# Kernel optimization log

Measured on AMD Instinct MI355X. Metric: run time of the kernel, lower is better.

Reference implementation:

```python
import jax, jax.numpy as jnp
import numpy as np

NUM_HEADS = 16  # init_kwargs num_heads


def setup_inputs() -> dict:
    key = jax.random.key(0)
    ks = jax.random.split(key, 3)
    B, S, D = 4, 2048, 1024
    scale = 1.0 / np.sqrt(D)
    return {
        "x": jax.random.normal(ks[0], (B, S, D), dtype=jnp.float32),
        "in_proj_w": jax.random.normal(ks[1], (3 * D, D), dtype=jnp.float32) * scale,
        "in_proj_b": jnp.zeros((3 * D,), dtype=jnp.float32),
        "out_w": jax.random.normal(ks[2], (D, D), dtype=jnp.float32) * scale,
        "out_b": jnp.zeros((D,), dtype=jnp.float32),
        "gamma": jnp.ones((D,), dtype=jnp.float32),
        "beta": jnp.zeros((D,), dtype=jnp.float32),
    }


def reference(x, in_proj_w, in_proj_b, out_w, out_b, gamma, beta):
    B, S, D = x.shape
    H = NUM_HEADS
    hd = D // H
    # packed qkv projection (torch Linear convention: y = x @ W.T + b)
    qkv = x @ in_proj_w.T + in_proj_b            # [B,S,3D]
    q, k, v = jnp.split(qkv, 3, axis=-1)
    q = q.reshape(B, S, H, hd).transpose(0, 2, 1, 3)  # [B,H,S,hd]
    k = k.reshape(B, S, H, hd).transpose(0, 2, 1, 3)
    v = v.reshape(B, S, H, hd).transpose(0, 2, 1, 3)

    scores = jnp.einsum("bhqd,bhkd->bhqk", q, k) / jnp.sqrt(jnp.asarray(hd, x.dtype))
    # additive causal mask: -inf above the diagonal
    causal = jnp.tril(jnp.ones((S, S), dtype=bool))
    scores = jnp.where(causal, scores, jnp.asarray(-jnp.inf, scores.dtype))
    attn = jax.nn.softmax(scores, axis=-1)       # [B,H,S,S]

    ctx = jnp.einsum("bhqk,bhkd->bhqd", attn, v)  # [B,H,S,hd]
    ctx = ctx.transpose(0, 2, 1, 3).reshape(B, S, D)
    attn_out = ctx @ out_w.T + out_b

    y = x + attn_out
    mu = jnp.mean(y, axis=-1, keepdims=True)
    var = jnp.mean(jnp.square(y - mu), axis=-1, keepdims=True)
    y = (y - mu) * jax.lax.rsqrt(var + 1e-5) * gamma + beta
    return y
```

## Files before the change

### kernel.cpp

```cpp
#include <hip/hip_runtime.h>
#include <stdint.h>

typedef unsigned short u16;
typedef __bf16 bf16x8 __attribute__((ext_vector_type(8)));
typedef float  f32x4  __attribute__((ext_vector_type(4)));
typedef int    i32x4  __attribute__((ext_vector_type(4)));

__device__ __forceinline__ u16 f2bf(float f){
  union{float f; uint32_t u;} v; v.f = f;
  uint32_t r = v.u + 0x7FFFu + ((v.u >> 16) & 1u);
  return (u16)(r >> 16);
}

#define GLDS16(gp, lp) __builtin_amdgcn_global_load_lds( \
    (const __attribute__((address_space(1))) void*)(gp),  \
    (__attribute__((address_space(3))) void*)(lp), 16, 0, 0)

__global__ __launch_bounds__(256) void cvt_kernel(const float* __restrict__ in,
                                                  u16* __restrict__ out, int n4) {
  int stride = gridDim.x * blockDim.x;
  for (int i = blockIdx.x * blockDim.x + threadIdx.x; i < n4; i += stride) {
    float4 v = ((const float4*)in)[i];
    u16 o0 = f2bf(v.x), o1 = f2bf(v.y), o2 = f2bf(v.z), o3 = f2bf(v.w);
    u16* p = out + (size_t)i * 4;
    uint32_t lo = (uint32_t)o0 | ((uint32_t)o1 << 16);
    uint32_t hi = (uint32_t)o2 | ((uint32_t)o3 << 16);
    ((uint2*)p)[0] = make_uint2(lo, hi);
  }
}

template <int MODE>
__global__ __launch_bounds__(256) void gemm_bt(
    const u16* __restrict__ A, const u16* __restrict__ B,
    const float* __restrict__ bias,
    u16* __restrict__ Cbf, float* __restrict__ Cf, const float* __restrict__ resid,
    int M, int N, int K) {
  __shared__ u16 Alds[128 * 32];
  __shared__ u16 Blds[128 * 32];
  const int t = threadIdx.x;
  const int w = t >> 6, l = t & 63;
  const int wr = w >> 1, wc = w & 1;
  const int g = l >> 4, r16 = l & 15;
  const int brow = blockIdx.y * 128, bcol = blockIdx.x * 128;

  f32x4 acc[4][4];
#pragma unroll
  for (int mi = 0; mi < 4; mi++)
#pragma unroll
    for (int nj = 0; nj < 4; nj++) acc[mi][nj] = (f32x4){0.f, 0.f, 0.f, 0.f};

  const int c0 = 2 * w, c1 = 2 * w + 1;
  const int srow0 = c0 * 16 + (l >> 2);
  const int srow1 = c1 * 16 + (l >> 2);
  const int scol = (l & 3) * 8;

  for (int kt = 0; kt < K; kt += 32) {
    __syncthreads();
    GLDS16(A + (size_t)(brow + srow0) * K + kt + scol, (char*)Alds + c0 * 1024);
    GLDS16(A + (size_t)(brow + srow1) * K + kt + scol, (char*)Alds + c1 * 1024);
    GLDS16(B + (size_t)(bcol + srow0) * K + kt + scol, (char*)Blds + c0 * 1024);
    GLDS16(B + (size_t)(bcol + srow1) * K + kt + scol, (char*)Blds + c1 * 1024);
    __syncthreads();

    bf16x8 af[4], bfr[4];
#pragma unroll
    for (int mi = 0; mi < 4; mi++)
      af[mi] = *(const bf16x8*)&Alds[(wr * 64 + mi * 16 + r16) * 32 + g * 8];
#pragma unroll
    for (int nj = 0; nj < 4; nj++)
      bfr[nj] = *(const bf16x8*)&Blds[(wc * 64 + nj * 16 + r16) * 32 + g * 8];
#pragma unroll
    for (int mi = 0; mi < 4; mi++)
#pragma unroll
      for (int nj = 0; nj < 4; nj++)
        acc[mi][nj] = __builtin_amdgcn_mfma_f32_16x16x32_bf16(af[mi], bfr[nj], acc[mi][nj], 0, 0, 0);
  }

#pragma unroll
  for (int mi = 0; mi < 4; mi++) {
#pragma unroll
    for (int nj = 0; nj < 4; nj++) {
      int col = bcol + wc * 64 + nj * 16 + r16;
      float bv = bias[col];
#pragma unroll
      for (int rr = 0; rr < 4; rr++) {
        int row = brow + wr * 64 + mi * 16 + g * 4 + rr;
        float v = acc[mi][nj][rr] + bv;
        if (MODE == 0) {
          Cbf[(size_t)row * N + col] = f2bf(v);
        } else {
          v += resid[(size_t)row * N + col];
          Cf[(size_t)row * N + col] = v;
        }
      }
    }
  }
}

__global__ __launch_bounds__(256) void vtrans_kernel(const u16* __restrict__ qkv,
                                                     u16* __restrict__ vtg) {
  const int S = 2048, HD3 = 3072;
  __shared__ u16 Vs[64 * 64];
  const int st = blockIdx.x, h = blockIdx.y, b = blockIdx.z;
  const int t = threadIdx.x;
  const int s0 = st * 64;
#pragma unroll
  for (int i = 0; i < 2; i++) {
    int n = t + i * 256;
    int row = n >> 3, c = n & 7;
    const u16* src = qkv + ((size_t)(b * S) + s0 + row) * HD3 + 2048 + h * 64 + c * 8;
    i32x4 v = *(const i32x4*)src;
    *(i32x4*)&Vs[row * 64 + ((c ^ (row & 7)) << 3)] = v;
  }
  __syncthreads();
  const int d = t >> 2;
  const int dc = d >> 3, dl = d & 7;
#pragma unroll
  for (int i = 0; i < 2; i++) {
    int kc = (t & 3) + i * 4;
    u16 tmp[8];
#pragma unroll
    for (int j = 0; j < 8; j++) {
      int k = kc * 8 + j;
      tmp[j] = Vs[k * 64 + ((dc ^ (k & 7)) << 3) + dl];
    }
    *(i32x4*)(vtg + ((size_t)(b * 16 + h) * 64 + d) * S + s0 + kc * 8) = *(i32x4*)tmp;
  }
}

__global__ __launch_bounds__(256) void attn_kernel(const u16* __restrict__ qkv,
                                                   const u16* __restrict__ vtg,
                                                   u16* __restrict__ ctxb) {
  const int S = 2048, HD3 = 3072;
  __shared__ u16 Kl[2][64 * 64];
  __shared__ u16 Vl[2][64 * 64];
  __shared__ u16 Pb[4][16 * 64];

  const int qi = 15 - (int)blockIdx.y;
  const int h = blockIdx.x & 15, b = blockIdx.x >> 4;
  const int t = threadIdx.x, w = t >> 6, l = t & 63;
  const int g = l >> 4, r16 = l & 15;
  const int q0 = qi * 128;
  const int nt = 2 * qi + 2;
  const size_t bS = (size_t)b * S;
  const size_t vbase = ((size_t)(b * 16 + h)) * 64 * S;

  const int q0w = q0 + w * 32;
  bf16x8 qf[2][2];
#pragma unroll
  for (int hh = 0; hh < 2; hh++) {
    const u16* qp = qkv + (bS + q0w + hh * 16 + r16) * HD3 + h * 64 + g * 8;
    qf[hh][0] = *(const bf16x8*)qp;
    qf[hh][1] = *(const bf16x8*)(qp + 32);
  }

  f32x4 ctx[2][4];
#pragma unroll
  for (int hh = 0; hh < 2; hh++)
#pragma unroll
    for (int f = 0; f < 4; f++) ctx[hh][f] = (f32x4){0.f, 0.f, 0.f, 0.f};
  float mrun[2] = {-1e30f, -1e30f};
  float lrun[2] = {0.f, 0.f};

#define STAGE(kt_, bi_)                                                        \
  do {                                                                         \
    const int k0s = (kt_) * 64;                                                \
    _Pragma("unroll")                                                          \
    for (int c = 0; c < 2; c++) {                                              \
      int n = c * 256 + t;                                                     \
      int row = n >> 3, sl = n & 7;                                            \
      int col = ((sl ^ (row & 7)) << 3);                                       \
      GLDS16(qkv + (bS + k0s + row) * HD3 + 1024 + h * 64 + col,               \
             (char*)&Kl[bi_][0] + c * 4096 + w * 1024);                        \
      GLDS16(vtg + vbase + (size_t)row * S + k0s + col,                        \
             (char*)&Vl[bi_][0] + c * 4096 + w * 1024);                        \
    }                                                                          \
  } while (0)

  STAGE(0, 0);
  int cur = 0;
  for (int kt = 0; kt < nt; kt++) {
    const int k0 = kt * 64;
    asm volatile("s_waitcnt vmcnt(0)" ::: "memory");
    __syncthreads();
    if (kt + 1 < nt) STAGE(kt + 1, cur ^ 1);

    bf16x8 kf[4][2];
#pragma unroll
    for (int f = 0; f < 4; f++) {
      int row = f * 16 + r16;
#pragma unroll
      for (int c = 0; c < 2; c++)
        kf[f][c] = *(const bf16x8*)&Kl[cur][row * 64 + (((c * 4 + g) ^ (row & 7)) << 3)];
    }

#pragma unroll
    for (int hh = 0; hh < 2; hh++) {
      const int qmin = q0w + hh * 16;
      if (k0 >= qmin + 16) continue;

      f32x4 sf[4];
#pragma unroll
      for (int f = 0; f < 4; f++) {
        f32x4 s = (f32x4){0.f, 0.f, 0.f, 0.f};
        s = __builtin_amdgcn_mfma_f32_16x16x32_bf16(kf[f][0], qf[hh][0], s, 0, 0, 0);
        s = __builtin_amdgcn_mfma_f32_16x16x32_bf16(kf[f][1], qf[hh][1], s, 0, 0, 0);
        sf[f] = s * 0.125f;
      }
      const int qg = qmin + r16;
      if (k0 + 64 > qmin) {
#pragma unroll
        for (int f = 0; f < 4; f++)
#pragma unroll
          for (int rr = 0; rr < 4; rr++)
            if (k0 + f * 16 + g * 4 + rr > qg) sf[f][rr] = -1e30f;
      }

      float tm = sf[0][0];
#pragma unroll
      for (int f = 0; f < 4; f++)
#pragma unroll
        for (int rr = 0; rr < 4; rr++) tm = fmaxf(tm, sf[f][rr]);
      tm = fmaxf(tm, __shfl_xor(tm, 16, 64));
      tm = fmaxf(tm, __shfl_xor(tm, 32, 64));

      float mold = mrun[hh];
      float mnew = fmaxf(mold, tm);
      mrun[hh] = mnew;

      float p[4][4];
      float ps = 0.f;
#pragma unroll
      for (int f = 0; f < 4; f++)
#pragma unroll
        for (int rr = 0; rr < 4; rr++) {
          p[f][rr] = __expf(sf[f][rr] - mnew);
          ps += p[f][rr];
        }
      ps += __shfl_xor(ps, 16, 64);
      ps += __shfl_xor(ps, 32, 64);
      float sc = __expf(mold - mnew);
      lrun[hh] = lrun[hh] * sc + ps;

#pragma unroll
      for (int f = 0; f < 4; f++)
#pragma unroll
        for (int rr2 = 0; rr2 < 4; rr2 += 2) {
          union { __bf16 b; u16 u; } a0, a1;
          a0.b = (__bf16)p[f][rr2];
          a1.b = (__bf16)p[f][rr2 + 1];
          uint32_t pk = (uint32_t)a0.u | ((uint32_t)a1.u << 16);
          int kidx = f * 16 + g * 4 + rr2;
          int ch = kidx >> 3;
          *(uint32_t*)((char*)&Pb[w][0] + r16 * 128 + ((ch ^ (r16 & 7)) << 4) +
                       ((kidx & 7) << 1)) = pk;
        }

#pragma unroll
      for (int rr = 0; rr < 4; rr++) {
        float scq = __shfl(sc, g * 4 + rr, 64);
#pragma unroll
        for (int f = 0; f < 4; f++) ctx[hh][f][rr] *= scq;
      }

      bf16x8 pf[2];
#pragma unroll
      for (int kh = 0; kh < 2; kh++)
        pf[kh] = *(const bf16x8*)((char*)&Pb[w][0] + r16 * 128 +
                                  (((kh * 4 + g) ^ (r16 & 7)) << 4));
#pragma unroll
      for (int f = 0; f < 4; f++) {
        int row = f * 16 + r16;
#pragma unroll
        for (int kh = 0; kh < 2; kh++) {
          bf16x8 vf = *(const bf16x8*)&Vl[cur][row * 64 + (((kh * 4 + g) ^ (row & 7)) << 3)];
          ctx[hh][f] = __builtin_amdgcn_mfma_f32_16x16x32_bf16(pf[kh], vf, ctx[hh][f], 0, 0, 0);
        }
      }
    }
    cur ^= 1;
  }

#pragma unroll
  for (int hh = 0; hh < 2; hh++) {
    float linv = 1.f / lrun[hh];
#pragma unroll
    for (int rr = 0; rr < 4; rr++) {
      float li = __shfl(linv, g * 4 + rr, 64);
      int qg = q0w + hh * 16 + g * 4 + rr;
#pragma unroll
      for (int f = 0; f < 4; f++) {
        union { __bf16 b; u16 u; } o;
        o.b = (__bf16)(ctx[hh][f][rr] * li);
        ctxb[(bS + qg) * 1024 + h * 64 + f * 16 + r16] = o.u;
      }
    }
  }
#undef STAGE
}

__global__ __launch_bounds__(256) void ln_kernel(float* __restrict__ y,
                                                 const float* __restrict__ gamma,
                                                 const float* __restrict__ beta) {
  __shared__ float sh[4];
  const int row = blockIdx.x, t = threadIdx.x;
  const int w = t >> 6, l = t & 63;
  float4 v = ((const float4*)(y + (size_t)row * 1024))[t];
  float s = v.x + v.y + v.z + v.w;
#pragma unroll
  for (int m = 32; m; m >>= 1) s += __shfl_xor(s, m, 64);
  if (l == 0) sh[w] = s;
  __syncthreads();
  float mu = (sh[0] + sh[1] + sh[2] + sh[3]) * (1.0f / 1024.0f);
  float dx = v.x - mu, dy = v.y - mu, dz = v.z - mu, dw = v.w - mu;
  float ss = dx * dx + dy * dy + dz * dz + dw * dw;
#pragma unroll
  for (int m = 32; m; m >>= 1) ss += __shfl_xor(ss, m, 64);
  __syncthreads();
  if (l == 0) sh[w] = ss;
  __syncthreads();
  float var = (sh[0] + sh[1] + sh[2] + sh[3]) * (1.0f / 1024.0f);
  float rs = rsqrtf(var + 1e-5f);
  float4 gm = ((const float4*)gamma)[t];
  float4 bt = ((const float4*)beta)[t];
  float4 o;
  o.x = dx * rs * gm.x + bt.x;
  o.y = dy * rs * gm.y + bt.y;
  o.z = dz * rs * gm.z + bt.z;
  o.w = dw * rs * gm.w + bt.w;
  ((float4*)(y + (size_t)row * 1024))[t] = o;
}

extern "C" void kernel_launch(void* const* d_in, const int* in_sizes, int n_in,
                              void* d_out, int out_size, void* d_ws, size_t ws_size,
                              hipStream_t stream) {
  (void)in_sizes; (void)n_in; (void)out_size; (void)ws_size;
  const float* x     = (const float*)d_in[0];
  const float* w1    = (const float*)d_in[1];
  const float* b1    = (const float*)d_in[2];
  const float* w2    = (const float*)d_in[3];
  const float* b2    = (const float*)d_in[4];
  const float* gamma = (const float*)d_in[5];
  const float* beta  = (const float*)d_in[6];
  float* out = (float*)d_out;

  const int M = 8192, D = 1024, N1 = 3072;

  char* ws = (char*)d_ws;
  u16* x_bf   = (u16*)(ws);
  u16* w1_bf  = (u16*)(ws + 16777216);
  u16* w2_bf  = (u16*)(ws + 23068672);
  u16* qkv_bf = (u16*)(ws + 25165824);
  u16* ctx_bf = (u16*)(ws + 75497472);
  u16* vtg    = (u16*)(ws);

  cvt_kernel<<<2048, 256, 0, stream>>>(x, x_bf, M * D / 4);
  cvt_kernel<<<1024, 256, 0, stream>>>(w1, w1_bf, N1 * D / 4);
  cvt_kernel<<<512, 256, 0, stream>>>(w2, w2_bf, D * D / 4);

  gemm_bt<0><<<dim3(N1 / 128, M / 128), 256, 0, stream>>>(
      x_bf, w1_bf, b1, qkv_bf, nullptr, nullptr, M, N1, D);

  vtrans_kernel<<<dim3(32, 16, 4), 256, 0, stream>>>(qkv_bf, vtg);

  attn_kernel<<<dim3(64, 16), 256, 0, stream>>>(qkv_bf, vtg, ctx_bf);

  gemm_bt<1><<<dim3(D / 128, M / 128), 256, 0, stream>>>(
      ctx_bf, w2_bf, b2, nullptr, out, x, M, D, D);

  ln_kernel<<<M, 256, 0, stream>>>(out, gamma, beta);
}
```

Measured before the change: 321.7 us.

## Pair causal query tiles per block, fold scale into Q, skip rescale, swizzle GEMM tiles

The attention grid is halved, and each block now processes two query tiles (pair and 15-pair) so causal work is balanced across blocks. The softmax scale and log2e are folded into Q once, so the loop can use exp2f. Rescaling of the accumulator is skipped when the running max grows by less than 8 (FA4-style lazy rescale). LDS offsets are precomputed, and the GEMM block index is XCD-swizzled for better L2 locality. Together these cut tail imbalance and per-tile ALU work, at the cost of extra bf16 rounding of Q and possible loss of fp32 headroom in the lazy-rescale path.

```diff
diff --git a/kernel.cpp b/kernel.cpp
--- a/kernel.cpp
+++ b/kernel.cpp
@@ -41,7 +41,13 @@
   const int w = t >> 6, l = t & 63;
   const int wr = w >> 1, wc = w & 1;
   const int g = l >> 4, r16 = l & 15;
-  const int brow = blockIdx.y * 128, bcol = blockIdx.x * 128;
+
+  const int gx = gridDim.x;
+  const int nwg = gx * gridDim.y;
+  const int wg = blockIdx.y * gx + blockIdx.x;
+  const int cpx = nwg >> 3;
+  const int swz = (wg & 7) * cpx + (wg >> 3);
+  const int brow = (swz / gx) * 128, bcol = (swz % gx) * 128;
 
   f32x4 acc[4][4];
 #pragma unroll
@@ -136,163 +142,190 @@
   __shared__ u16 Vl[2][64 * 64];
   __shared__ u16 Pb[4][16 * 64];
 
-  const int qi = 15 - (int)blockIdx.y;
   const int h = blockIdx.x & 15, b = blockIdx.x >> 4;
+  const int pair = blockIdx.y;
   const int t = threadIdx.x, w = t >> 6, l = t & 63;
   const int g = l >> 4, r16 = l & 15;
-  const int q0 = qi * 128;
-  const int nt = 2 * qi + 2;
   const size_t bS = (size_t)b * S;
   const size_t vbase = ((size_t)(b * 16 + h)) * 64 * S;
 
-  const int q0w = q0 + w * 32;
-  bf16x8 qf[2][2];
-#pragma unroll
-  for (int hh = 0; hh < 2; hh++) {
-    const u16* qp = qkv + (bS + q0w + hh * 16 + r16) * HD3 + h * 64 + g * 8;
-    qf[hh][0] = *(const bf16x8*)qp;
-    qf[hh][1] = *(const bf16x8*)(qp + 32);
-  }
-
-  f32x4 ctx[2][4];
-#pragma unroll
-  for (int hh = 0; hh < 2; hh++)
-#pragma unroll
-    for (int f = 0; f < 4; f++) ctx[hh][f] = (f32x4){0.f, 0.f, 0.f, 0.f};
-  float mrun[2] = {-1e30f, -1e30f};
-  float lrun[2] = {0.f, 0.f};
-
-#define STAGE(kt_, bi_)                                                        \
-  do {                                                                         \
-    const int k0s = (kt_) * 64;                                                \
-    _Pragma("unroll")                                                          \
-    for (int c = 0; c < 2; c++) {                                              \
-      int n = c * 256 + t;                                                     \
-      int row = n >> 3, sl = n & 7;                                            \
-      int col = ((sl ^ (row & 7)) << 3);                                       \
-      GLDS16(qkv + (bS + k0s + row) * HD3 + 1024 + h * 64 + col,               \
-             (char*)&Kl[bi_][0] + c * 4096 + w * 1024);                        \
-      GLDS16(vtg + vbase + (size_t)row * S + k0s + col,                        \
-             (char*)&Vl[bi_][0] + c * 4096 + w * 1024);                        \
-    }                                                                          \
+  const int srow = t >> 3, ssl = t & 7;
+  const int scol = ((ssl ^ (srow & 7)) << 3);
+  const int sdst = w * 1024;
+
+  int kfo[4][2], pwo[4][2], pro[2];
+#pragma unroll
+  for (int f = 0; f < 4; f++) {
+    int row = f * 16 + r16;
+#pragma unroll
+    for (int c = 0; c < 2; c++)
+      kfo[f][c] = (row * 64 + (((c * 4 + g) ^ (row & 7)) << 3)) * 2;
+#pragma unroll
+    for (int q2 = 0; q2 < 2; q2++) {
+      int kidx = f * 16 + g * 4 + q2 * 2;
+      pwo[f][q2] = r16 * 128 + (((kidx >> 3) ^ (r16 & 7)) << 4) + ((kidx & 7) << 1);
+    }
+  }
+#pragma unroll
+  for (int kh = 0; kh < 2; kh++)
+    pro[kh] = r16 * 128 + (((kh * 4 + g) ^ (r16 & 7)) << 4);
+
+  const float QSC = 0.125f * 1.44269504f;
+
+#define STAGE(bi_)                                                            \
+  do {                                                                        \
+    GLDS16(kp, (char*)Kl + (bi_)*8192 + sdst);                                \
+    GLDS16(kp + 32 * HD3, (char*)Kl + (bi_)*8192 + 4096 + sdst);              \
+    GLDS16(vp, (char*)Vl + (bi_)*8192 + sdst);                                \
+    GLDS16(vp + 32 * S, (char*)Vl + (bi_)*8192 + 4096 + sdst);                \
+    kp += 64 * HD3; vp += 64;                                                 \
   } while (0)
 
-  STAGE(0, 0);
-  int cur = 0;
-  for (int kt = 0; kt < nt; kt++) {
-    const int k0 = kt * 64;
-    asm volatile("s_waitcnt vmcnt(0)" ::: "memory");
+  for (int seg = 0; seg < 2; seg++) {
+    const int qi = seg ? (15 - pair) : pair;
+    const int q0w = qi * 128 + w * 32;
+    const int nt = 2 * qi + 2;
+
+    bf16x8 qf[2][2];
+#pragma unroll
+    for (int hh = 0; hh < 2; hh++) {
+      const u16* qp = qkv + (bS + q0w + hh * 16 + r16) * HD3 + h * 64 + g * 8;
+      bf16x8 a = *(const bf16x8*)qp;
+      bf16x8 c = *(const bf16x8*)(qp + 32);
+#pragma unroll
+      for (int j = 0; j < 8; j++) {
+        a[j] = (__bf16)((float)a[j] * QSC);
+        c[j] = (__bf16)((float)c[j] * QSC);
+      }
+      qf[hh][0] = a; qf[hh][1] = c;
+    }
+
+    f32x4 ctx[2][4];
+#pragma unroll
+    for (int hh = 0; hh < 2; hh++)
+#pragma unroll
+      for (int f = 0; f < 4; f++) ctx[hh][f] = (f32x4){0.f, 0.f, 0.f, 0.f};
+    float mrun[2] = {-1e30f, -1e30f};
+    float lrun[2] = {0.f, 0.f};
+
+    const u16* kp = qkv + (bS + srow) * HD3 + 1024 + h * 64 + scol;
+    const u16* vp = vtg + vbase + (size_t)srow * S + scol;
+
     __syncthreads();
-    if (kt + 1 < nt) STAGE(kt + 1, cur ^ 1);
-
-    bf16x8 kf[4][2];
-#pragma unroll
-    for (int f = 0; f < 4; f++) {
-      int row = f * 16 + r16;
-#pragma unroll
-      for (int c = 0; c < 2; c++)
-        kf[f][c] = *(const bf16x8*)&Kl[cur][row * 64 + (((c * 4 + g) ^ (row & 7)) << 3)];
+    STAGE(0);
+    int cur = 0;
+    for (int kt = 0; kt < nt; kt++) {
+      const int k0 = kt * 64;
+      asm volatile("s_waitcnt vmcnt(0)" ::: "memory");
+      __syncthreads();
+      if (kt + 1 < nt) STAGE(cur ^ 1);
+
+      const char* KB = (const char*)Kl + cur * 8192;
+      const char* VB = (const char*)Vl + cur * 8192;
+      bf16x8 kf[4][2];
+#pragma unroll
+      for (int f = 0; f < 4; f++)
+#pragma unroll
+        for (int c = 0; c < 2; c++) kf[f][c] = *(const bf16x8*)(KB + kfo[f][c]);
+
+#pragma unroll
+      for (int hh = 0; hh < 2; hh++) {
+        const int qmin = q0w + hh * 16;
+        if (k0 >= qmin + 16) continue;
+
+        f32x4 sf[4];
+#pragma unroll
+        for (int f = 0; f < 4; f++) {
+          f32x4 s = (f32x4){0.f, 0.f, 0.f, 0.f};
+          s = __builtin_amdgcn_mfma_f32_16x16x32_bf16(kf[f][0], qf[hh][0], s, 0, 0, 0);
+          s = __builtin_amdgcn_mfma_f32_16x16x32_bf16(kf[f][1], qf[hh][1], s, 0, 0, 0);
+          sf[f] = s;
+        }
+        const int qg = qmin + r16;
+        if (k0 + 64 > qmin) {
+#pragma unroll
+          for (int f = 0; f < 4; f++)
+#pragma unroll
+            for (int rr = 0; rr < 4; rr++)
+              if (k0 + f * 16 + g * 4 + rr > qg) sf[f][rr] = -1e30f;
+        }
+
+        float tm = sf[0][0];
+#pragma unroll
+        for (int f = 0; f < 4; f++)
+#pragma unroll
+          for (int rr = 0; rr < 4; rr++) tm = fmaxf(tm, sf[f][rr]);
+        tm = fmaxf(tm, __shfl_xor(tm, 16, 64));
+        tm = fmaxf(tm, __shfl_xor(tm, 32, 64));
+
+        const float mold = mrun[hh];
+        const bool skip = __all(tm <= mold + 8.0f);
+        const float mnew = skip ? mold : fmaxf(mold, tm);
+        mrun[hh] = mnew;
+
+        float p[4][4];
+        float ps = 0.f;
+#pragma unroll
+        for (int f = 0; f < 4; f++)
+#pragma unroll
+          for (int rr = 0; rr < 4; rr++) {
+            p[f][rr] = exp2f(sf[f][rr] - mnew);
+            ps += p[f][rr];
+          }
+        ps += __shfl_xor(ps, 16, 64);
+        ps += __shfl_xor(ps, 32, 64);
+
+        if (skip) {
+          lrun[hh] += ps;
+        } else {
+          float sc = exp2f(mold - mnew);
+          lrun[hh] = lrun[hh] * sc + ps;
+#pragma unroll
+          for (int rr = 0; rr < 4; rr++) {
+            float scq = __shfl(sc, g * 4 + rr, 64);
+#pragma unroll
+            for (int f = 0; f < 4; f++) ctx[hh][f][rr] *= scq;
+          }
+        }
+
+        char* PW = (char*)Pb + w * 2048;
+#pragma unroll
+        for (int f = 0; f < 4; f++)
+#pragma unroll
+          for (int q2 = 0; q2 < 2; q2++) {
+            union { __bf16 b; u16 u; } a0, a1;
+            a0.b = (__bf16)p[f][q2 * 2];
+            a1.b = (__bf16)p[f][q2 * 2 + 1];
+            *(uint32_t*)(PW + pwo[f][q2]) = (uint32_t)a0.u | ((uint32_t)a1.u << 16);
+          }
+
+        bf16x8 pf[2];
+#pragma unroll
+        for (int kh = 0; kh < 2; kh++) pf[kh] = *(const bf16x8*)(PW + pro[kh]);
+#pragma unroll
+        for (int f = 0; f < 4; f++)
+#pragma unroll
+          for (int kh = 0; kh < 2; kh++) {
+            bf16x8 vf = *(const bf16x8*)(VB + kfo[f][kh]);
+            ctx[hh][f] = __builtin_amdgcn_mfma_f32_16x16x32_bf16(pf[kh], vf, ctx[hh][f], 0, 0, 0);
+          }
+      }
+      cur ^= 1;
     }
 
 #pragma unroll
     for (int hh = 0; hh < 2; hh++) {
-      const int qmin = q0w + hh * 16;
-      if (k0 >= qmin + 16) continue;
-
-      f32x4 sf[4];
-#pragma unroll
-      for (int f = 0; f < 4; f++) {
-        f32x4 s = (f32x4){0.f, 0.f, 0.f, 0.f};
-        s = __builtin_amdgcn_mfma_f32_16x16x32_bf16(kf[f][0], qf[hh][0], s, 0, 0, 0);
-        s = __builtin_amdgcn_mfma_f32_16x16x32_bf16(kf[f][1], qf[hh][1], s, 0, 0, 0);
-        sf[f] = s * 0.125f;
-      }
-      const int qg = qmin + r16;
-      if (k0 + 64 > qmin) {
-#pragma unroll
-        for (int f = 0; f < 4; f++)
-#pragma unroll
-          for (int rr = 0; rr < 4; rr++)
-            if (k0 + f * 16 + g * 4 + rr > qg) sf[f][rr] = -1e30f;
-      }
-
-      float tm = sf[0][0];
-#pragma unroll
-      for (int f = 0; f < 4; f++)
-#pragma unroll
-        for (int rr = 0; rr < 4; rr++) tm = fmaxf(tm, sf[f][rr]);
-      tm = fmaxf(tm, __shfl_xor(tm, 16, 64));
-      tm = fmaxf(tm, __shfl_xor(tm, 32, 64));
-
-      float mold = mrun[hh];
-      float mnew = fmaxf(mold, tm);
-      mrun[hh] = mnew;
-
-      float p[4][4];
-      float ps = 0.f;
-#pragma unroll
-      for (int f = 0; f < 4; f++)
-#pragma unroll
-        for (int rr = 0; rr < 4; rr++) {
-          p[f][rr] = __expf(sf[f][rr] - mnew);
-          ps += p[f][rr];
+      float linv = 1.f / lrun[hh];
+#pragma unroll
+      for (int rr = 0; rr < 4; rr++) {
+        float li = __shfl(linv, g * 4 + rr, 64);
+        int qg = q0w + hh * 16 + g * 4 + rr;
+#pragma unroll
+        for (int f = 0; f < 4; f++) {
+          union { __bf16 b; u16 u; } o;
+          o.b = (__bf16)(ctx[hh][f][rr] * li);
+          ctxb[(bS + qg) * 1024 + h * 64 + f * 16 + r16] = o.u;
         }
-      ps += __shfl_xor(ps, 16, 64);
-      ps += __shfl_xor(ps, 32, 64);
-      float sc = __expf(mold - mnew);
-      lrun[hh] = lrun[hh] * sc + ps;
-
-#pragma unroll
-      for (int f = 0; f < 4; f++)
-#pragma unroll
-        for (int rr2 = 0; rr2 < 4; rr2 += 2) {
-          union { __bf16 b; u16 u; } a0, a1;
-          a0.b = (__bf16)p[f][rr2];
-          a1.b = (__bf16)p[f][rr2 + 1];
-          uint32_t pk = (uint32_t)a0.u | ((uint32_t)a1.u << 16);
-          int kidx = f * 16 + g * 4 + rr2;
-          int ch = kidx >> 3;
-          *(uint32_t*)((char*)&Pb[w][0] + r16 * 128 + ((ch ^ (r16 & 7)) << 4) +
-                       ((kidx & 7) << 1)) = pk;
-        }
-
-#pragma unroll
-      for (int rr = 0; rr < 4; rr++) {
-        float scq = __shfl(sc, g * 4 + rr, 64);
-#pragma unroll
-        for (int f = 0; f < 4; f++) ctx[hh][f][rr] *= scq;
-      }
-
-      bf16x8 pf[2];
-#pragma unroll
-      for (int kh = 0; kh < 2; kh++)
-        pf[kh] = *(const bf16x8*)((char*)&Pb[w][0] + r16 * 128 +
-                                  (((kh * 4 + g) ^ (r16 & 7)) << 4));
-#pragma unroll
-      for (int f = 0; f < 4; f++) {
-        int row = f * 16 + r16;
-#pragma unroll
-        for (int kh = 0; kh < 2; kh++) {
-          bf16x8 vf = *(const bf16x8*)&Vl[cur][row * 64 + (((kh * 4 + g) ^ (row & 7)) << 3)];
-          ctx[hh][f] = __builtin_amdgcn_mfma_f32_16x16x32_bf16(pf[kh], vf, ctx[hh][f], 0, 0, 0);
-        }
-      }
-    }
-    cur ^= 1;
-  }
-
-#pragma unroll
-  for (int hh = 0; hh < 2; hh++) {
-    float linv = 1.f / lrun[hh];
-#pragma unroll
-    for (int rr = 0; rr < 4; rr++) {
-      float li = __shfl(linv, g * 4 + rr, 64);
-      int qg = q0w + hh * 16 + g * 4 + rr;
-#pragma unroll
-      for (int f = 0; f < 4; f++) {
-        union { __bf16 b; u16 u; } o;
-        o.b = (__bf16)(ctx[hh][f][rr] * li);
-        ctxb[(bS + qg) * 1024 + h * 64 + f * 16 + r16] = o.u;
       }
     }
   }
@@ -363,7 +396,7 @@
 
   vtrans_kernel<<<dim3(32, 16, 4), 256, 0, stream>>>(qkv_bf, vtg);
 
-  attn_kernel<<<dim3(64, 16), 256, 0, stream>>>(qkv_bf, vtg, ctx_bf);
+  attn_kernel<<<dim3(64, 8), 256, 0, stream>>>(qkv_bf, vtg, ctx_bf);
 
   gemm_bt<1><<<dim3(D / 128, M / 128), 256, 0, stream>>>(
       ctx_bf, w2_bf, b2, nullptr, out, x, M, D, D);
```

New measurement: 318.6 us. No clear change (-1.0%).
